# Kernel optimization log

Hardware: AMD Instinct MI355X
Metric: run time of the kernel (lower is better)

Reference implementation:

```python
import jax, jax.numpy as jnp
import numpy as np

B, NX, NY = 4, 16384, 16384
CX = CY = 256
CK = CV = 256
H = 8


def setup_inputs() -> dict:
    key = jax.random.key(0)
    ks = jax.random.split(key, 12)
    s = 0.02
    return {
        "x": jax.random.normal(ks[0], (B, NX, CX), jnp.float32),
        "y": jax.random.normal(ks[1], (B, NY, CY), jnp.float32),
        "x_pos_embed": jax.random.normal(ks[2], (B, NX, CX), jnp.float32),
        "y_pos_embed": jax.random.normal(ks[3], (B, NY, CY), jnp.float32),
        "Wq": jax.random.normal(ks[4], (CK, CX), jnp.float32) * s,
        "bq": jnp.zeros((CK,), jnp.float32),
        "Wk": jax.random.normal(ks[5], (CK, CY), jnp.float32) * s,
        "bk": jnp.zeros((CK,), jnp.float32),
        "Wv": jax.random.normal(ks[6], (CV, CY), jnp.float32) * s,
        "bv": jnp.zeros((CV,), jnp.float32),
        "Wr": jax.random.normal(ks[7], (CX, CV), jnp.float32) * s,
        "br": jnp.zeros((CX,), jnp.float32),
    }


def reference(x, y, x_pos_embed, y_pos_embed, Wq, bq, Wk, bk, Wv, bv, Wr, br):
    # Linear projections (nn.Linear: x @ W.T + b)
    q = (x + x_pos_embed) @ Wq.T + bq            # [B, Nx, Ck]
    k = (y + y_pos_embed) @ Wk.T + bk            # [B, Ny, Ck]
    v = y @ Wv.T + bv                            # [B, Ny, Cv]

    dk, dv = CK // H, CV // H
    # Split heads: [B, N, H, d] -> [B, H, N, d]
    q = q.reshape(B, NX, H, dk).transpose(0, 2, 1, 3)
    k = k.reshape(B, NY, H, dk).transpose(0, 2, 1, 3)
    v = v.reshape(B, NY, H, dv).transpose(0, 2, 1, 3)

    # key softmax over tokens (Ny); query softmax over per-head channels (dk)
    k = jax.nn.softmax(k, axis=2)                # [B, H, Ny, dk]
    q = jax.nn.softmax(q, axis=3)                # [B, H, Nx, dk]

    # context = softmax(K)^T V : [B, H, dk, dv]
    context = jnp.einsum('bhnk,bhnv->bhkv', k, v)
    # attended = Q context : [B, H, Nx, dv]
    attended = jnp.einsum('bhnk,bhkv->bhnv', q, context)

    # merge heads -> [B, Nx, Cv], reproject -> [B, Nx, Cx]
    agg = attended.transpose(0, 2, 1, 3).reshape(B, NX, CV)
    return agg @ Wr.T + br
```

## Files before the change

kernel.cpp:

```cpp
#include <hip/hip_runtime.h>


typedef float f32x4 __attribute__((ext_vector_type(4)));
typedef short s16x4 __attribute__((ext_vector_type(4)));
typedef short s16x8 __attribute__((ext_vector_type(8)));

#define MFMA16(A, B, C) __builtin_amdgcn_mfma_f32_16x16x32_bf16((A), (B), (C), 0, 0, 0)

__device__ __forceinline__ short f2bf(float f) {
    unsigned u = __builtin_bit_cast(unsigned, f);
    u = (u + 0x7FFFu + ((u >> 16) & 1u)) >> 16;
    return (short)u;
}
__device__ __forceinline__ float bf2f(short b) {
    unsigned u = ((unsigned)(unsigned short)b) << 16;
    return __builtin_bit_cast(float, u);
}

__global__ __launch_bounds__(256) void wcvt_kernel(
    const float* __restrict__ wq, const float* __restrict__ wk,
    const float* __restrict__ wv, const float* __restrict__ wr,
    short* __restrict__ wbf)
{
    int id = blockIdx.x * 256 + threadIdx.x;
    int m = id >> 13;
    int slot = id & 8191;
    int tile = slot >> 9;
    int ks   = (slot >> 6) & 7;
    int lane = slot & 63;
    int lrow = lane & 15, lgrp = lane >> 4;
    const float* src = (m == 0) ? wq : (m == 1) ? wk : (m == 2) ? wv : wr;
    const float* p = src + (size_t)(tile * 16 + lrow) * 256 + ks * 32 + lgrp * 8;
    f32x4 a = *(const f32x4*)p;
    f32x4 b = *(const f32x4*)(p + 4);
    s16x8 o;
    o[0]=f2bf(a[0]); o[1]=f2bf(a[1]); o[2]=f2bf(a[2]); o[3]=f2bf(a[3]);
    o[4]=f2bf(b[0]); o[5]=f2bf(b[1]); o[6]=f2bf(b[2]); o[7]=f2bf(b[3]);
    *(s16x8*)(wbf + (size_t)id * 8) = o;
}

__global__ __launch_bounds__(512, 4) void kv_kernel(
    const float* __restrict__ y, const float* __restrict__ ypos,
    const short* __restrict__ wkp, const short* __restrict__ wvp,
    const float* __restrict__ bk, const float* __restrict__ bv,
    short* __restrict__ e_buf, short* __restrict__ v_buf)
{
    __shared__ short ak[64 * 256];
    __shared__ short av[64 * 256];
    const int row0 = blockIdx.x * 64;
    const int t = threadIdx.x;
    const int w = t >> 6, lane = t & 63;

    {
        #pragma unroll
        for (int it = 0; it < 8; ++it) {
            int r = it * 8 + w;
            const float* sy = y    + (size_t)(row0 + r) * 256 + lane * 4;
            const float* sp = ypos + (size_t)(row0 + r) * 256 + lane * 4;
            f32x4 a = *(const f32x4*)sy;
            f32x4 p = *(const f32x4*)sp;
            f32x4 k = a + p;
            s16x4 ov, ok;
            ov[0]=f2bf(a[0]); ov[1]=f2bf(a[1]); ov[2]=f2bf(a[2]); ov[3]=f2bf(a[3]);
            ok[0]=f2bf(k[0]); ok[1]=f2bf(k[1]); ok[2]=f2bf(k[2]); ok[3]=f2bf(k[3]);
            int swz = ((lane >> 1) ^ (r & 7)) * 8 + (lane & 1) * 4;
            *(s16x4*)(av + r * 256 + swz) = ov;
            *(s16x4*)(ak + r * 256 + swz) = ok;
        }
    }
    __syncthreads();

    const int lrow = lane & 15, lgrp = lane >> 4;
    const bool is_k = (w < 4);
    const int wrow0 = ((w >> 1) & 1) * 32;
    const int colbase = (w & 1) * 128;
    const short* WP = is_k ? wkp : wvp;
    const float* bp = is_k ? bk : bv;
    short* obuf = is_k ? e_buf : v_buf;
    const short* A = is_k ? ak : av;

    float bias[8];
    #pragma unroll
    for (int nf = 0; nf < 8; ++nf) bias[nf] = bp[colbase + nf * 16 + lrow];

    s16x8 af[2][8];
    #pragma unroll
    for (int mf = 0; mf < 2; ++mf) {
        int rr = wrow0 + mf * 16 + lrow;
        #pragma unroll
        for (int ks = 0; ks < 8; ++ks) {
            int cs = ((ks * 4 + lgrp) ^ (rr & 7));
            af[mf][ks] = *(const s16x8*)(A + rr * 256 + cs * 8);
        }
    }

    #pragma unroll
    for (int nf = 0; nf < 8; ++nf) {
        const int tile = (colbase >> 4) + nf;
        const short* wt = WP + ((size_t)tile * 8) * 512 + lane * 8;
        f32x4 a0 = (f32x4){0.f, 0.f, 0.f, 0.f};
        f32x4 a1 = (f32x4){0.f, 0.f, 0.f, 0.f};
        #pragma unroll
        for (int kg = 0; kg < 2; ++kg) {
            s16x8 bf[4];
            #pragma unroll
            for (int kk = 0; kk < 4; ++kk)
                bf[kk] = *(const s16x8*)(wt + (kg * 4 + kk) * 512);
            #pragma unroll
            for (int kk = 0; kk < 4; ++kk) {
                a0 = MFMA16(af[0][kg * 4 + kk], bf[kk], a0);
                a1 = MFMA16(af[1][kg * 4 + kk], bf[kk], a1);
            }
        }
        const int col = colbase + nf * 16 + lrow;
        #pragma unroll
        for (int rr = 0; rr < 4; ++rr) {
            int g0 = row0 + wrow0 + lgrp * 4 + rr;
            float v0 = a0[rr] + bias[nf];
            float v1 = a1[rr] + bias[nf];
            if (is_k) { v0 = __expf(v0); v1 = __expf(v1); }
            obuf[(size_t)g0 * 256 + col]        = f2bf(v0);
            obuf[(size_t)(g0 + 16) * 256 + col] = f2bf(v1);
        }
    }
}

__global__ __launch_bounds__(256) void ctx_kernel(
    const short* __restrict__ e_buf, const short* __restrict__ v_buf,
    float* __restrict__ partials)
{
    __shared__ float se[128 * 32];
    __shared__ float sv[128 * 32];
    __shared__ float red[4 * 1056];
    const int cb = blockIdx.x, bh = blockIdx.y;
    const int b = bh >> 3, h = bh & 7;
    const int tok0 = b * 16384 + cb * 1024;
    const int t = threadIdx.x, w = t >> 6, lane = t & 63;
    const int ckb = (lane >> 3) * 4, cvb = (lane & 7) * 4;

    f32x4 acc[4];
    #pragma unroll
    for (int i = 0; i < 4; ++i) acc[i] = (f32x4){0.f, 0.f, 0.f, 0.f};
    f32x4 dn = (f32x4){0.f, 0.f, 0.f, 0.f};

    for (int it = 0; it < 8; ++it) {
        __syncthreads();
        #pragma unroll
        for (int s = 0; s < 2; ++s) {
            int id = t + s * 256;
            int rr = id >> 2, pp = id & 3;
            size_t g = (size_t)(tok0 + it * 128 + rr) * 256 + h * 32 + pp * 8;
            s16x8 ee = *(const s16x8*)(e_buf + g);
            s16x8 vv = *(const s16x8*)(v_buf + g);
            f32x4 e0 = {bf2f(ee[0]), bf2f(ee[1]), bf2f(ee[2]), bf2f(ee[3])};
            f32x4 e1 = {bf2f(ee[4]), bf2f(ee[5]), bf2f(ee[6]), bf2f(ee[7])};
            f32x4 v0 = {bf2f(vv[0]), bf2f(vv[1]), bf2f(vv[2]), bf2f(vv[3])};
            f32x4 v1 = {bf2f(vv[4]), bf2f(vv[5]), bf2f(vv[6]), bf2f(vv[7])};
            *(f32x4*)(se + rr * 32 + pp * 8)     = e0;
            *(f32x4*)(se + rr * 32 + pp * 8 + 4) = e1;
            *(f32x4*)(sv + rr * 32 + pp * 8)     = v0;
            *(f32x4*)(sv + rr * 32 + pp * 8 + 4) = v1;
        }
        __syncthreads();
        const int r0 = w * 32;
        #pragma unroll 8
        for (int rr = 0; rr < 32; ++rr) {
            f32x4 e4 = *(const f32x4*)(se + (r0 + rr) * 32 + ckb);
            f32x4 v4 = *(const f32x4*)(sv + (r0 + rr) * 32 + cvb);
            acc[0] += e4[0] * v4;
            acc[1] += e4[1] * v4;
            acc[2] += e4[2] * v4;
            acc[3] += e4[3] * v4;
            dn += e4;
        }
    }
    __syncthreads();
    #pragma unroll
    for (int i = 0; i < 4; ++i)
        *(f32x4*)(red + w * 1056 + (ckb + i) * 32 + cvb) = acc[i];
    if ((lane & 7) == 0)
        *(f32x4*)(red + w * 1056 + 1024 + ckb) = dn;
    __syncthreads();
    float* outp = partials + (size_t)(bh * 16 + cb) * 1056;
    for (int e = t; e < 1056; e += 256)
        outp[e] = red[e] + red[1056 + e] + red[2112 + e] + red[3168 + e];
}

__global__ __launch_bounds__(256) void ctx_reduce_kernel(
    const float* __restrict__ partials, short* __restrict__ ctxT)
{
    __shared__ float s[1056];
    const int bh = blockIdx.x, t = threadIdx.x;
    for (int e = t; e < 1056; e += 256) {
        float a = 0.f;
        for (int c = 0; c < 16; ++c) a += partials[(size_t)(bh * 16 + c) * 1056 + e];
        s[e] = a;
    }
    __syncthreads();
    for (int e = t; e < 1024; e += 256) {
        int ck = e >> 5, cv = e & 31;
        float val = s[e] / s[1024 + ck];
        ctxT[(size_t)bh * 1024 + cv * 32 + ck] = f2bf(val);
    }
}

__global__ __launch_bounds__(256, 4) void qout_kernel(
    const float* __restrict__ x, const float* __restrict__ xpos,
    const short* __restrict__ wqp, const float* __restrict__ bq,
    const short* __restrict__ ctxT,
    const short* __restrict__ wrp, const float* __restrict__ br,
    float* __restrict__ out)
{
    __shared__ short alds[32 * 256];
    __shared__ short qlds[4][32 * 64];
    const int row0 = blockIdx.x * 32;
    const int b = row0 >> 14;
    const int t = threadIdx.x;
    const int w = t >> 6, lane = t & 63;

    {
        #pragma unroll
        for (int it = 0; it < 8; ++it) {
            int r = it * 4 + w;
            const float* sx = x    + (size_t)(row0 + r) * 256 + lane * 4;
            const float* sp = xpos + (size_t)(row0 + r) * 256 + lane * 4;
            f32x4 a = *(const f32x4*)sx;
            f32x4 p = *(const f32x4*)sp;
            a += p;
            s16x4 o;
            o[0]=f2bf(a[0]); o[1]=f2bf(a[1]); o[2]=f2bf(a[2]); o[3]=f2bf(a[3]);
            int swz = ((lane >> 1) ^ (r & 7)) * 8 + (lane & 1) * 4;
            *(s16x4*)(alds + r * 256 + swz) = o;
        }
    }
    __syncthreads();

    const int lrow = lane & 15, lgrp = lane >> 4;
    const int wc = w * 64;

    float biasq[4];
    #pragma unroll
    for (int nf = 0; nf < 4; ++nf) biasq[nf] = bq[wc + nf * 16 + lrow];

    f32x4 acc[2][4];
    #pragma unroll
    for (int mf = 0; mf < 2; ++mf)
        #pragma unroll
        for (int nf = 0; nf < 4; ++nf) acc[mf][nf] = (f32x4){0.f, 0.f, 0.f, 0.f};

    #pragma unroll
    for (int ks = 0; ks < 8; ++ks) {
        s16x8 af[2];
        #pragma unroll
        for (int mf = 0; mf < 2; ++mf) {
            int rr = mf * 16 + lrow;
            int cs = (ks * 4 + lgrp) ^ (rr & 7);
            af[mf] = *(const s16x8*)(alds + rr * 256 + cs * 8);
        }
        #pragma unroll
        for (int nf = 0; nf < 4; ++nf) {
            int tile = (wc >> 4) + nf;
            s16x8 bfr = *(const s16x8*)(wqp + ((size_t)tile * 8 + ks) * 512 + lane * 8);
            acc[0][nf] = MFMA16(af[0], bfr, acc[0][nf]);
            acc[1][nf] = MFMA16(af[1], bfr, acc[1][nf]);
        }
    }

    short* ql = (short*)qlds[w];
    #pragma unroll
    for (int mf = 0; mf < 2; ++mf) {
        f32x4 e[4];
        #pragma unroll
        for (int nf = 0; nf < 4; ++nf)
            #pragma unroll
            for (int rr = 0; rr < 4; ++rr)
                e[nf][rr] = __expf(acc[mf][nf][rr] + biasq[nf]);
        #pragma unroll
        for (int hl = 0; hl < 2; ++hl) {
            #pragma unroll
            for (int rr = 0; rr < 4; ++rr) {
                float s = e[hl * 2][rr] + e[hl * 2 + 1][rr];
                s += __shfl_xor(s, 1);
                s += __shfl_xor(s, 2);
                s += __shfl_xor(s, 4);
                s += __shfl_xor(s, 8);
                float rinv = 1.0f / s;
                int row = mf * 16 + lgrp * 4 + rr;
                #pragma unroll
                for (int n2 = 0; n2 < 2; ++n2) {
                    int colc = hl * 32 + n2 * 16 + lrow;
                    int cs = (colc >> 3) ^ (row & 7);
                    ql[row * 64 + cs * 8 + (colc & 7)] = f2bf(e[hl * 2 + n2][rr] * rinv);
                }
            }
        }
    }
    __syncthreads();

    f32x4 att[2][2][2];
    #pragma unroll
    for (int hl = 0; hl < 2; ++hl)
        #pragma unroll
        for (int mf = 0; mf < 2; ++mf)
            #pragma unroll
            for (int n2 = 0; n2 < 2; ++n2) att[hl][mf][n2] = (f32x4){0.f,0.f,0.f,0.f};

    #pragma unroll
    for (int hl = 0; hl < 2; ++hl) {
        const short* cbase = ctxT + (size_t)(b * 8 + w * 2 + hl) * 1024;
        s16x8 bctx[2];
        #pragma unroll
        for (int n2 = 0; n2 < 2; ++n2)
            bctx[n2] = *(const s16x8*)(cbase + (n2 * 16 + lrow) * 32 + lgrp * 8);
        #pragma unroll
        for (int mf = 0; mf < 2; ++mf) {
            int row = mf * 16 + lrow;
            int cs = (hl * 4 + lgrp) ^ (row & 7);
            s16x8 aq = *(const s16x8*)(ql + row * 64 + cs * 8);
            #pragma unroll
            for (int n2 = 0; n2 < 2; ++n2)
                att[hl][mf][n2] = MFMA16(aq, bctx[n2], att[hl][mf][n2]);
        }
    }

    #pragma unroll
    for (int hl = 0; hl < 2; ++hl)
      #pragma unroll
      for (int mf = 0; mf < 2; ++mf)
        #pragma unroll
        for (int n2 = 0; n2 < 2; ++n2)
          #pragma unroll
          for (int rr = 0; rr < 4; ++rr) {
              int row = mf * 16 + lgrp * 4 + rr;
              int col = wc + hl * 32 + n2 * 16 + lrow;
              int cs = (col >> 3) ^ (row & 7);
              alds[row * 256 + cs * 8 + (col & 7)] = f2bf(att[hl][mf][n2][rr]);
          }
    __syncthreads();

    float biasr[4];
    #pragma unroll
    for (int nf = 0; nf < 4; ++nf) biasr[nf] = br[wc + nf * 16 + lrow];

    f32x4 acc2[2][4];
    #pragma unroll
    for (int mf = 0; mf < 2; ++mf)
        #pragma unroll
        for (int nf = 0; nf < 4; ++nf) acc2[mf][nf] = (f32x4){0.f, 0.f, 0.f, 0.f};

    #pragma unroll
    for (int ks = 0; ks < 8; ++ks) {
        s16x8 af[2];
        #pragma unroll
        for (int mf = 0; mf < 2; ++mf) {
            int rr = mf * 16 + lrow;
            int cs = (ks * 4 + lgrp) ^ (rr & 7);
            af[mf] = *(const s16x8*)(alds + rr * 256 + cs * 8);
        }
        #pragma unroll
        for (int nf = 0; nf < 4; ++nf) {
            int tile = (wc >> 4) + nf;
            s16x8 bfr = *(const s16x8*)(wrp + ((size_t)tile * 8 + ks) * 512 + lane * 8);
            acc2[0][nf] = MFMA16(af[0], bfr, acc2[0][nf]);
            acc2[1][nf] = MFMA16(af[1], bfr, acc2[1][nf]);
        }
    }

    #pragma unroll
    for (int mf = 0; mf < 2; ++mf)
      #pragma unroll
      for (int nf = 0; nf < 4; ++nf)
        #pragma unroll
        for (int rr = 0; rr < 4; ++rr) {
            int grow = row0 + mf * 16 + lgrp * 4 + rr;
            out[(size_t)grow * 256 + wc + nf * 16 + lrow] = acc2[mf][nf][rr] + biasr[nf];
        }
}

extern "C" void kernel_launch(void* const* d_in, const int* in_sizes, int n_in,
                              void* d_out, int out_size, void* d_ws, size_t ws_size,
                              hipStream_t stream)
{
    const float* x    = (const float*)d_in[0];
    const float* y    = (const float*)d_in[1];
    const float* xpos = (const float*)d_in[2];
    const float* ypos = (const float*)d_in[3];
    const float* Wq   = (const float*)d_in[4];
    const float* bq   = (const float*)d_in[5];
    const float* Wk   = (const float*)d_in[6];
    const float* bk   = (const float*)d_in[7];
    const float* Wv   = (const float*)d_in[8];
    const float* bv   = (const float*)d_in[9];
    const float* Wr   = (const float*)d_in[10];
    const float* br   = (const float*)d_in[11];

    char*  ws    = (char*)d_ws;
    short* wbf   = (short*)(ws);
    short* ctxT  = (short*)(ws + 524288);
    float* parts = (float*)(ws + (1 << 20));
    short* e_buf = (short*)(ws + ((size_t)4 << 20));
    short* v_buf = e_buf + (size_t)65536 * 256;
    float* outp  = (float*)d_out;

    hipLaunchKernelGGL(wcvt_kernel, dim3(128), dim3(256), 0, stream,
                       Wq, Wk, Wv, Wr, wbf);
    hipLaunchKernelGGL(kv_kernel, dim3(1024), dim3(512), 0, stream,
                       y, ypos, wbf + 65536, wbf + 131072, bk, bv, e_buf, v_buf);
    hipLaunchKernelGGL(ctx_kernel, dim3(16, 32), dim3(256), 0, stream,
                       e_buf, v_buf, parts);
    hipLaunchKernelGGL(ctx_reduce_kernel, dim3(32), dim3(256), 0, stream,
                       parts, ctxT);
    hipLaunchKernelGGL(qout_kernel, dim3(2048), dim3(256), 0, stream,
                       x, xpos, wbf, bq, ctxT, wbf + 196608, br, outp);
}
```

Baseline: 169.9 us.

## Stage kv projection outputs in LDS for coalesced 16-byte global stores

The kv kernel now handles 32 rows per 256-thread block instead of 64 rows per 512-thread block. It reuses the input LDS buffer to stage the exp(K) and V bf16 results in a swizzled layout, then writes them out as full-row 16-byte vector stores. This replaces the earlier scattered 2-byte global stores, which wrote poorly coalesced output. The cost is an extra LDS round trip, two more barriers, and smaller blocks, which change occupancy and weight-load reuse.

```diff
diff --git a/kernel.cpp b/kernel.cpp
--- a/kernel.cpp
+++ b/kernel.cpp
@@ -39,22 +39,23 @@
     *(s16x8*)(wbf + (size_t)id * 8) = o;
 }
 
-__global__ __launch_bounds__(512, 4) void kv_kernel(
+__global__ __launch_bounds__(256, 4) void kv_kernel(
     const float* __restrict__ y, const float* __restrict__ ypos,
     const short* __restrict__ wkp, const short* __restrict__ wvp,
     const float* __restrict__ bk, const float* __restrict__ bv,
     short* __restrict__ e_buf, short* __restrict__ v_buf)
 {
-    __shared__ short ak[64 * 256];
-    __shared__ short av[64 * 256];
-    const int row0 = blockIdx.x * 64;
+    __shared__ short smem[32 * 512];
+    short* ak = smem;
+    short* av = smem + 32 * 256;
+    const int row0 = blockIdx.x * 32;
     const int t = threadIdx.x;
     const int w = t >> 6, lane = t & 63;
 
     {
         #pragma unroll
         for (int it = 0; it < 8; ++it) {
-            int r = it * 8 + w;
+            int r = it * 4 + w;
             const float* sy = y    + (size_t)(row0 + r) * 256 + lane * 4;
             const float* sp = ypos + (size_t)(row0 + r) * 256 + lane * 4;
             f32x4 a = *(const f32x4*)sy;
@@ -71,12 +72,10 @@
     __syncthreads();
 
     const int lrow = lane & 15, lgrp = lane >> 4;
-    const bool is_k = (w < 4);
-    const int wrow0 = ((w >> 1) & 1) * 32;
+    const bool is_k = (w < 2);
     const int colbase = (w & 1) * 128;
     const short* WP = is_k ? wkp : wvp;
     const float* bp = is_k ? bk : bv;
-    short* obuf = is_k ? e_buf : v_buf;
     const short* A = is_k ? ak : av;
 
     float bias[8];
@@ -86,13 +85,14 @@
     s16x8 af[2][8];
     #pragma unroll
     for (int mf = 0; mf < 2; ++mf) {
-        int rr = wrow0 + mf * 16 + lrow;
+        int rr = mf * 16 + lrow;
         #pragma unroll
         for (int ks = 0; ks < 8; ++ks) {
             int cs = ((ks * 4 + lgrp) ^ (rr & 7));
             af[mf][ks] = *(const s16x8*)(A + rr * 256 + cs * 8);
         }
     }
+    __syncthreads();
 
     #pragma unroll
     for (int nf = 0; nf < 8; ++nf) {
@@ -112,15 +112,30 @@
                 a1 = MFMA16(af[1][kg * 4 + kk], bf[kk], a1);
             }
         }
-        const int col = colbase + nf * 16 + lrow;
+        const int colp = (is_k ? 0 : 256) + colbase + nf * 16 + lrow;
         #pragma unroll
         for (int rr = 0; rr < 4; ++rr) {
-            int g0 = row0 + wrow0 + lgrp * 4 + rr;
             float v0 = a0[rr] + bias[nf];
             float v1 = a1[rr] + bias[nf];
             if (is_k) { v0 = __expf(v0); v1 = __expf(v1); }
-            obuf[(size_t)g0 * 256 + col]        = f2bf(v0);
-            obuf[(size_t)(g0 + 16) * 256 + col] = f2bf(v1);
+            int lr0 = lgrp * 4 + rr;
+            int lr1 = lr0 + 16;
+            smem[lr0 * 512 + (((colp >> 3) ^ (lr0 & 7)) * 8) + (colp & 7)] = f2bf(v0);
+            smem[lr1 * 512 + (((colp >> 3) ^ (lr1 & 7)) * 8) + (colp & 7)] = f2bf(v1);
+        }
+    }
+    __syncthreads();
+
+    {
+        #pragma unroll
+        for (int i = 0; i < 8; ++i) {
+            int r = i * 4 + w;
+            int grow = row0 + r;
+            s16x8 val = *(const s16x8*)(smem + r * 512 + (lane ^ (r & 7)) * 8);
+            if (lane < 32)
+                *(s16x8*)(e_buf + (size_t)grow * 256 + lane * 8) = val;
+            else
+                *(s16x8*)(v_buf + (size_t)grow * 256 + (lane - 32) * 8) = val;
         }
     }
 }
@@ -404,7 +419,7 @@
 
     hipLaunchKernelGGL(wcvt_kernel, dim3(128), dim3(256), 0, stream,
                        Wq, Wk, Wv, Wr, wbf);
-    hipLaunchKernelGGL(kv_kernel, dim3(1024), dim3(512), 0, stream,
+    hipLaunchKernelGGL(kv_kernel, dim3(2048), dim3(256), 0, stream,
                        y, ypos, wbf + 65536, wbf + 131072, bk, bv, e_buf, v_buf);
     hipLaunchKernelGGL(ctx_kernel, dim3(16, 32), dim3(256), 0, stream,
                        e_buf, v_buf, parts);
```

Result: no change. 169.1 us (-0.5%).
